# Performance work log

Hardware: AMD Instinct MI355X
Metric: run time of the kernel (lower is better)

## Reference

```python
import jax, jax.numpy as jnp
import numpy as np

B, S, D_IN, D_OUT, H = 2, 2048, 1024, 1024, 16
HD = D_OUT // H

def setup_inputs() -> dict:
    key = jax.random.key(0)
    ks = jax.random.split(key, 6)
    sc_in = 1.0 / np.sqrt(D_IN)
    sc_out = 1.0 / np.sqrt(D_OUT)
    return {
        "x": jax.random.normal(ks[0], (B, S, D_IN), dtype=jnp.float32),
        "Wq": jax.random.uniform(ks[1], (D_IN, D_OUT), jnp.float32, -sc_in, sc_in),
        "Wk": jax.random.uniform(ks[2], (D_IN, D_OUT), jnp.float32, -sc_in, sc_in),
        "Wv": jax.random.uniform(ks[3], (D_IN, D_OUT), jnp.float32, -sc_in, sc_in),
        "Wo": jax.random.uniform(ks[4], (D_OUT, D_OUT), jnp.float32, -sc_out, sc_out),
        "bo": jax.random.uniform(ks[5], (D_OUT,), jnp.float32, -sc_out, sc_out),
    }

def reference(x, Wq, Wk, Wv, Wo, bo):
    b, s, _ = x.shape
    # QKV projections (no bias), split heads -> [b, h, s, hd]
    q = (x @ Wq).reshape(b, s, H, HD).transpose(0, 2, 1, 3)
    k = (x @ Wk).reshape(b, s, H, HD).transpose(0, 2, 1, 3)
    v = (x @ Wv).reshape(b, s, H, HD).transpose(0, 2, 1, 3)
    scores = jnp.einsum('bhqd,bhkd->bhqk', q, k)
    causal = jnp.triu(jnp.ones((s, s), dtype=bool), k=1)
    scores = jnp.where(causal, -jnp.inf, scores)
    w = jax.nn.softmax(scores / np.sqrt(HD), axis=-1)  # dropout p=0.0 -> identity
    ctx = jnp.einsum('bhqk,bhkd->bhqd', w, v)
    ctx = ctx.transpose(0, 2, 1, 3).reshape(b, s, D_OUT)
    return ctx @ Wo + bo
```

## Files before the change

### kernel.cpp

```cpp
#include <hip/hip_runtime.h>
#include <stdint.h>

typedef unsigned short u16;
typedef __attribute__((ext_vector_type(8))) short short8;
typedef __attribute__((ext_vector_type(4))) float floatx4;
typedef __attribute__((ext_vector_type(4))) u16 ushort4v;

typedef __attribute__((address_space(1))) const uint32_t gu32;
typedef __attribute__((address_space(3))) uint32_t lu32;

#define MFMA(a, b, c) __builtin_amdgcn_mfma_f32_16x16x32_bf16((a), (b), (c), 0, 0, 0)

__device__ __forceinline__ u16 f2bf(float f) {
    union { float f; uint32_t u; } x; x.f = f;
    uint32_t u = x.u;
    u += 0x7fffu + ((u >> 16) & 1u);
    return (u16)(u >> 16);
}

__device__ __forceinline__ uint32_t cvtpk_bf16(float lo, float hi) {
    uint32_t r;
    asm("v_cvt_pk_bf16_f32 %0, %1, %2" : "=v"(r) : "v"(lo), "v"(hi));
    return r;
}

__device__ __forceinline__ float fexp2(float x) {
#if defined(__has_builtin)
#if __has_builtin(__builtin_amdgcn_exp2f)
    return __builtin_amdgcn_exp2f(x);
#else
    return exp2f(x);
#endif
#else
    return exp2f(x);
#endif
}

__device__ __forceinline__ void async16(u16* lds, const u16* g) {
    __builtin_amdgcn_global_load_lds((gu32*)g, (lu32*)lds, 16, 0, 0);
}

#define KV8(buf, row, byteInRow) \
    (*(short8*)((char*)(buf) + (((row) << 7) + ((byteInRow) ^ (((row) & 7) << 4)))))

#define Q_SCALE_LOG2E 0.18033688011112042f

__global__ __launch_bounds__(256) void prep_kernel(
    const float* __restrict__ x,
    const float* __restrict__ W0, const float* __restrict__ W1,
    const float* __restrict__ W2, const float* __restrict__ W3,
    u16* __restrict__ WT, u16* __restrict__ Xbf)
{
    const int z = blockIdx.z;
    const int tx = threadIdx.x, ty = threadIdx.y;
    if (z == 4) {
        const int bid = blockIdx.y * 32 + blockIdx.x;
        const int t = ty * 32 + tx;
        const size_t base = ((size_t)bid * 256 + t) * 16;
        const float* xf = x + base;
        short8 v0, v1;
#pragma unroll
        for (int j = 0; j < 8; j++) v0[j] = (short)f2bf(xf[j]);
#pragma unroll
        for (int j = 0; j < 8; j++) v1[j] = (short)f2bf(xf[8 + j]);
        *(short8*)&Xbf[base] = v0;
        *(short8*)&Xbf[base + 8] = v1;
        return;
    }
    __shared__ u16 tile[32][33];
    const float* W = (z == 0) ? W0 : (z == 1) ? W1 : (z == 2) ? W2 : W3;
    u16* dst = WT + (size_t)z * 1024 * 1024;
    const int n0 = blockIdx.x * 32, k0 = blockIdx.y * 32;
#pragma unroll
    for (int i = 0; i < 4; i++)
        tile[ty + i * 8][tx] = f2bf(W[(size_t)(k0 + ty + i * 8) * 1024 + n0 + tx]);
    __syncthreads();
#pragma unroll
    for (int i = 0; i < 4; i++)
        dst[(size_t)(n0 + ty + i * 8) * 1024 + k0 + tx] = tile[tx][ty + i * 8];
}

#define RSTAGE(Abuf, Bbuf, kk) do { \
    async16((Abuf) + (wave * 128) * 8,      gA0 + (kk)); \
    async16((Abuf) + (wave * 128 + 64) * 8, gA1 + (kk)); \
    async16((Bbuf) + (wave * 128) * 8,      gB0 + (kk)); \
    async16((Bbuf) + (wave * 128 + 64) * 8, gB1 + (kk)); \
} while (0)

#define GCOMPUTE(AB, BB) do { \
    short8 af[4], bfv[4]; \
    _Pragma("unroll") \
    for (int mt = 0; mt < 4; mt++) \
        af[mt] = *(const short8*)&(AB)[(wr + mt * 16 + lrow) * 32 + lquad * 8]; \
    _Pragma("unroll") \
    for (int nt = 0; nt < 4; nt++) \
        bfv[nt] = *(const short8*)&(BB)[(wc + nt * 16 + lrow) * 32 + lquad * 8]; \
    _Pragma("unroll") \
    for (int mt = 0; mt < 4; mt++) \
        _Pragma("unroll") \
        for (int nt = 0; nt < 4; nt++) \
            acc[mt][nt] = MFMA(af[mt], bfv[nt], acc[mt][nt]); \
} while (0)

#define RING_K_LOOP() do { \
    RSTAGE(As[0], Bs[0], 0); \
    RSTAGE(As[1], Bs[1], 32); \
    RSTAGE(As[2], Bs[2], 64); \
    for (int t = 0; t < 30; ++t) { \
        asm volatile("s_waitcnt vmcnt(8)" ::: "memory"); \
        __builtin_amdgcn_s_barrier(); \
        __builtin_amdgcn_sched_barrier(0); \
        if (t < 29) RSTAGE(As[(t + 3) & 3], Bs[(t + 3) & 3], (t + 3) * 32); \
        GCOMPUTE(As[t & 3], Bs[t & 3]); \
    } \
    asm volatile("s_waitcnt vmcnt(4)" ::: "memory"); \
    __builtin_amdgcn_s_barrier(); \
    __builtin_amdgcn_sched_barrier(0); \
    GCOMPUTE(As[2], Bs[2]); \
    asm volatile("s_waitcnt vmcnt(0)" ::: "memory"); \
    __builtin_amdgcn_s_barrier(); \
    __builtin_amdgcn_sched_barrier(0); \
    GCOMPUTE(As[3], Bs[3]); \
} while (0)

__global__ __launch_bounds__(256) void gemm_qkv_kernel(
    const u16* __restrict__ X, const u16* __restrict__ WT,
    u16* __restrict__ Q, u16* __restrict__ Kout, u16* __restrict__ VT)
{
    __shared__ __align__(16) u16 As[4][128 * 32];
    __shared__ __align__(16) u16 Bs[4][128 * 32];
    const int bid = blockIdx.x;
    const int xcd = bid & 7;
    const int idx = bid >> 3;
    const int mat = idx >> 5;
    const int rr  = (idx >> 3) & 3;
    const int nn  = idx & 7;
    const int m0 = (xcd * 4 + rr) * 128;
    const int n0 = nn * 128;
    const u16* BW = WT + (size_t)mat * 1024 * 1024;
    const int tid = threadIdx.x;
    const int wave = tid >> 6, lane = tid & 63;
    const int lrow = lane & 15, lquad = lane >> 4;
    const int wr = (wave >> 1) * 64, wc = (wave & 1) * 64;

    const int ci0 = wave * 128 + lane;
    const int ci1 = ci0 + 64;
    const int ar0 = ci0 >> 2, ac0 = (ci0 & 3) * 8;
    const int ar1 = ci1 >> 2, ac1 = (ci1 & 3) * 8;
    const u16* gA0 = &X[(size_t)(m0 + ar0) * 1024 + ac0];
    const u16* gA1 = &X[(size_t)(m0 + ar1) * 1024 + ac1];
    const u16* gB0 = &BW[(size_t)(n0 + ar0) * 1024 + ac0];
    const u16* gB1 = &BW[(size_t)(n0 + ar1) * 1024 + ac1];

    floatx4 acc[4][4];
#pragma unroll
    for (int mt = 0; mt < 4; mt++)
#pragma unroll
        for (int nt = 0; nt < 4; nt++) acc[mt][nt] = (floatx4){0.f, 0.f, 0.f, 0.f};

    RING_K_LOOP();

    const float qs = (mat == 0) ? Q_SCALE_LOG2E : 1.0f;
#pragma unroll
    for (int mt = 0; mt < 4; mt++) {
        const int gm = m0 + wr + mt * 16 + lquad * 4;
        const int b_ = gm >> 11;
        const int s  = gm & 2047;
#pragma unroll
        for (int nt = 0; nt < 4; nt++) {
            const int gn = n0 + wc + nt * 16 + lrow;
            const int h = gn >> 6, hd = gn & 63;
            const int bh = b_ * 16 + h;
            if (mat == 2) {
                ushort4v v;
#pragma unroll
                for (int i = 0; i < 4; i++) v[i] = f2bf(acc[mt][nt][i]);
                *(ushort4v*)&VT[((size_t)bh * 64 + hd) * 2048 + s] = v;
            } else {
                u16* dst = (mat == 0) ? Q : Kout;
#pragma unroll
                for (int i = 0; i < 4; i++)
                    dst[((size_t)bh * 2048 + s + i) * 64 + hd] = f2bf(acc[mt][nt][i] * qs);
            }
        }
    }
}

__global__ __launch_bounds__(256, 4) void attn_kernel(
    const u16* __restrict__ Q, const u16* __restrict__ Kk,
    const u16* __restrict__ VT, u16* __restrict__ ctx)
{
    __shared__ __align__(16) u16 Ks[64 * 64];
    __shared__ __align__(16) u16 Vs[64 * 64];
    __shared__ __align__(16) u16 P[4][16][80];
    const int tid = threadIdx.x, wave = tid >> 6, lane = tid & 63;
    const int lrow = lane & 15, lquad = lane >> 4;
    const float NEGINF = -__builtin_inff();

    const int bh = blockIdx.x & 31;
    const int g = blockIdx.x >> 5;
    const int qb = (g < 16) ? (31 - g) : (g - 16);
    const int ntiles = qb + 1;
    const int q0 = qb * 64 + wave * 16;

    const u16* Qb = Q  + (size_t)bh * 2048 * 64;
    const u16* Kb = Kk + (size_t)bh * 2048 * 64;
    const u16* Vb = VT + (size_t)bh * 64 * 2048;

    const short8 qf0 = *(const short8*)&Qb[(size_t)(q0 + lrow) * 64 + lquad * 8];
    const short8 qf1 = *(const short8*)&Qb[(size_t)(q0 + lrow) * 64 + 32 + lquad * 8];

    const int myq = q0 + lrow;
    float m_s = NEGINF, l_s = 0.f;
    floatx4 o[4];
#pragma unroll
    for (int i = 0; i < 4; i++) o[i] = (floatx4){0.f, 0.f, 0.f, 0.f};

    const int r0 = tid >> 3, r1 = r0 + 32;
    const int ce = (tid & 7) * 8;
    const int cb = (tid & 7) * 16;

    short8 kreg0 = *(const short8*)&Kb[(size_t)r0 * 64 + ce];
    short8 kreg1 = *(const short8*)&Kb[(size_t)r1 * 64 + ce];
    short8 vreg0 = *(const short8*)&Vb[(size_t)r0 * 2048 + ce];
    short8 vreg1 = *(const short8*)&Vb[(size_t)r1 * 2048 + ce];

    for (int kt = 0; kt < ntiles; kt++) {
        __syncthreads();
        KV8(Ks, r0, cb) = kreg0;
        KV8(Ks, r1, cb) = kreg1;
        KV8(Vs, r0, cb) = vreg0;
        KV8(Vs, r1, cb) = vreg1;
        if (kt + 1 < ntiles) {
            kreg0 = *(const short8*)&Kb[(size_t)((kt + 1) * 64 + r0) * 64 + ce];
            kreg1 = *(const short8*)&Kb[(size_t)((kt + 1) * 64 + r1) * 64 + ce];
            vreg0 = *(const short8*)&Vb[(size_t)r0 * 2048 + (kt + 1) * 64 + ce];
            vreg1 = *(const short8*)&Vb[(size_t)r1 * 2048 + (kt + 1) * 64 + ce];
        }
        __syncthreads();

        floatx4 s[4];
#pragma unroll
        for (int nt = 0; nt < 4; nt++) {
            const short8 kf0 = KV8(Ks, nt * 16 + lrow, lquad * 16);
            const short8 kf1 = KV8(Ks, nt * 16 + lrow, 64 + lquad * 16);
            floatx4 a = (floatx4){0.f, 0.f, 0.f, 0.f};
            a = MFMA(kf0, qf0, a);
            a = MFMA(kf1, qf1, a);
            s[nt] = a;
        }

        if (kt == ntiles - 1) {
#pragma unroll
            for (int nt = 0; nt < 4; nt++)
#pragma unroll
                for (int i = 0; i < 4; i++)
                    if (kt * 64 + nt * 16 + lquad * 4 + i > myq) s[nt][i] = NEGINF;
        }

        float mx = NEGINF;
#pragma unroll
        for (int nt = 0; nt < 4; nt++)
            mx = fmaxf(mx, fmaxf(fmaxf(s[nt][0], s[nt][1]),
                                 fmaxf(s[nt][2], s[nt][3])));
        mx = fmaxf(mx, __shfl_xor(mx, 16));
        mx = fmaxf(mx, __shfl_xor(mx, 32));

        if (!__all(mx <= m_s + 8.0f)) {
            const float mnew = fmaxf(m_s, mx);
            const float alpha = fexp2(m_s - mnew);
            m_s = mnew;
            l_s *= alpha;
#pragma unroll
            for (int ht = 0; ht < 4; ht++)
#pragma unroll
                for (int i = 0; i < 4; i++) o[ht][i] *= alpha;
        }

        float sum = 0.f;
#pragma unroll
        for (int nt = 0; nt < 4; nt++)
#pragma unroll
            for (int i = 0; i < 4; i++) {
                const float pv = fexp2(s[nt][i] - m_s);
                s[nt][i] = pv;
                sum += pv;
            }
        sum += __shfl_xor(sum, 16);
        sum += __shfl_xor(sum, 32);
        l_s += sum;

#pragma unroll
        for (int nt = 0; nt < 4; nt++) {
            uint2 pk;
            pk.x = cvtpk_bf16(s[nt][0], s[nt][1]);
            pk.y = cvtpk_bf16(s[nt][2], s[nt][3]);
            *(uint2*)&P[wave][lrow][nt * 16 + lquad * 4] = pk;
        }
#pragma unroll
        for (int st = 0; st < 2; st++) {
            const short8 pf = *(const short8*)&P[wave][lrow][st * 32 + lquad * 8];
#pragma unroll
            for (int ht = 0; ht < 4; ht++) {
                const short8 vf = KV8(Vs, ht * 16 + lrow, st * 64 + lquad * 16);
                o[ht] = MFMA(vf, pf, o[ht]);
            }
        }
    }

    const int b_ = bh >> 4, h_ = bh & 15;
    const float inv_l = 1.0f / l_s;
#pragma unroll
    for (int ht = 0; ht < 4; ht++) {
        uint2 pk;
        pk.x = cvtpk_bf16(o[ht][0] * inv_l, o[ht][1] * inv_l);
        pk.y = cvtpk_bf16(o[ht][2] * inv_l, o[ht][3] * inv_l);
        *(uint2*)&ctx[((size_t)(b_ * 2048 + q0 + lrow)) * 1024 + h_ * 64 + ht * 16 + lquad * 4] = pk;
    }
}

__global__ __launch_bounds__(256) void gemm_out_kernel(
    const u16* __restrict__ X, const u16* __restrict__ WT,
    const float* __restrict__ bias, float* __restrict__ out)
{
    __shared__ __align__(16) u16 As[4][128 * 32];
    __shared__ __align__(16) u16 Bs[4][128 * 32];
    const int bid = blockIdx.x;
    const int xcd = bid & 7;
    const int idx = bid >> 3;
    const int rr  = idx >> 3;
    const int nn  = idx & 7;
    const int m0 = (xcd * 4 + rr) * 128;
    const int n0 = nn * 128;
    const int tid = threadIdx.x;
    const int wave = tid >> 6, lane = tid & 63;
    const int lrow = lane & 15, lquad = lane >> 4;
    const int wr = (wave >> 1) * 64, wc = (wave & 1) * 64;

    const int ci0 = wave * 128 + lane;
    const int ci1 = ci0 + 64;
    const int ar0 = ci0 >> 2, ac0 = (ci0 & 3) * 8;
    const int ar1 = ci1 >> 2, ac1 = (ci1 & 3) * 8;
    const u16* gA0 = &X[(size_t)(m0 + ar0) * 1024 + ac0];
    const u16* gA1 = &X[(size_t)(m0 + ar1) * 1024 + ac1];
    const u16* gB0 = &WT[(size_t)(n0 + ar0) * 1024 + ac0];
    const u16* gB1 = &WT[(size_t)(n0 + ar1) * 1024 + ac1];

    floatx4 acc[4][4];
#pragma unroll
    for (int mt = 0; mt < 4; mt++)
#pragma unroll
        for (int nt = 0; nt < 4; nt++) acc[mt][nt] = (floatx4){0.f, 0.f, 0.f, 0.f};

    RING_K_LOOP();

#pragma unroll
    for (int mt = 0; mt < 4; mt++) {
        const int gm = m0 + wr + mt * 16 + lquad * 4;
#pragma unroll
        for (int nt = 0; nt < 4; nt++) {
            const int gn = n0 + wc + nt * 16 + lrow;
            const float bv = bias[gn];
#pragma unroll
            for (int i = 0; i < 4; i++)
                out[(size_t)(gm + i) * 1024 + gn] = acc[mt][nt][i] + bv;
        }
    }
}

extern "C" void kernel_launch(void* const* d_in, const int* in_sizes, int n_in,
                              void* d_out, int out_size, void* d_ws, size_t ws_size,
                              hipStream_t stream) {
    u16* ws = (u16*)d_ws + 64;

    const size_t MB1 = 1024 * 1024;
    u16* WT   = ws;
    u16* Qw   = ws + 4 * MB1;
    u16* Kw   = ws + 8 * MB1;
    u16* VTw  = ws + 12 * MB1;
    u16* ctxw = ws + 16 * MB1;
    u16* Xbf  = ws + 20 * MB1;

    prep_kernel<<<dim3(32, 32, 5), dim3(32, 8), 0, stream>>>(
        (const float*)d_in[0], (const float*)d_in[1], (const float*)d_in[2],
        (const float*)d_in[3], (const float*)d_in[4], WT, Xbf);
    gemm_qkv_kernel<<<768, 256, 0, stream>>>(Xbf, WT, Qw, Kw, VTw);
    attn_kernel<<<1024, 256, 0, stream>>>(Qw, Kw, VTw, ctxw);
    gemm_out_kernel<<<256, 256, 0, stream>>>(ctxw, WT + 3 * MB1, (const float*)d_in[5], (float*)d_out);
}
```

Before: 192.7 us.

## Enlarge QKV GEMM tiles to 256x256 with swizzled LDS and 8 waves

```diff
diff --git a/kernel.cpp b/kernel.cpp
--- a/kernel.cpp
+++ b/kernel.cpp
@@ -78,6 +78,263 @@
 #pragma unroll
     for (int i = 0; i < 4; i++)
         dst[(size_t)(n0 + ty + i * 8) * 1024 + k0 + tx] = tile[tx][ty + i * 8];
+}
+
+__global__ __launch_bounds__(512, 2) void gemm_qkv_kernel(
+    const u16* __restrict__ X, const u16* __restrict__ WT,
+    u16* __restrict__ Q, u16* __restrict__ Kout, u16* __restrict__ VT)
+{
+    __shared__ __align__(16) u16 As[4][256 * 32];
+    __shared__ __align__(16) u16 Bs[4][256 * 32];
+    const int bid = blockIdx.x;
+    const int xcd = bid & 7;
+    const int idx = bid >> 3;
+    const int rr  = idx & 1;
+    const int nn  = idx >> 1;
+    const int m0 = (xcd * 2 + rr) * 256;
+    const int n0 = nn * 256;
+    const int tid = threadIdx.x;
+    const int wave = tid >> 6, lane = tid & 63;
+    const int lrow = lane & 15, lquad = lane >> 4;
+    const int wr = (wave >> 2) * 128;
+    const int wc = (wave & 3) * 64;
+
+    const int c0 = wave * 128 + lane;
+    const int c1 = c0 + 64;
+    const int row0 = c0 >> 2, row1 = c1 >> 2;
+    const int gc0 = (((c0 & 3) ^ (row0 & 3)) * 8);
+    const int gc1 = (((c1 & 3) ^ (row1 & 3)) * 8);
+    const u16* gA0 = &X[(size_t)(m0 + row0) * 1024 + gc0];
+    const u16* gA1 = &X[(size_t)(m0 + row1) * 1024 + gc1];
+    const u16* gB0 = &WT[(size_t)(n0 + row0) * 1024 + gc0];
+    const u16* gB1 = &WT[(size_t)(n0 + row1) * 1024 + gc1];
+    const int ldsOff0 = (wave * 128) * 8;
+    const int ldsOff1 = (wave * 128 + 64) * 8;
+
+#define QSTAGE(b, kk) do { \
+    async16(&As[b][ldsOff0], gA0 + (kk)); \
+    async16(&As[b][ldsOff1], gA1 + (kk)); \
+    async16(&Bs[b][ldsOff0], gB0 + (kk)); \
+    async16(&Bs[b][ldsOff1], gB1 + (kk)); \
+} while (0)
+
+    const int sb = (lquad * 16) ^ ((lrow & 3) << 4);
+
+    floatx4 acc[8][4];
+#pragma unroll
+    for (int mt = 0; mt < 8; mt++)
+#pragma unroll
+        for (int nt = 0; nt < 4; nt++) acc[mt][nt] = (floatx4){0.f, 0.f, 0.f, 0.f};
+
+#define QCOMPUTE(b) do { \
+    const char* ab = (const char*)As[b]; \
+    const char* bb = (const char*)Bs[b]; \
+    short8 af[8], bf01[2], bf23[2]; \
+    _Pragma("unroll") \
+    for (int mt = 0; mt < 8; mt++) \
+        af[mt] = *(const short8*)(ab + (wr + mt * 16 + lrow) * 64 + sb); \
+    _Pragma("unroll") \
+    for (int nt = 0; nt < 2; nt++) \
+        bf01[nt] = *(const short8*)(bb + (wc + nt * 16 + lrow) * 64 + sb); \
+    __builtin_amdgcn_s_setprio(1); \
+    _Pragma("unroll") \
+    for (int mt = 0; mt < 8; mt++) { \
+        acc[mt][0] = MFMA(af[mt], bf01[0], acc[mt][0]); \
+        acc[mt][1] = MFMA(af[mt], bf01[1], acc[mt][1]); \
+    } \
+    __builtin_amdgcn_s_setprio(0); \
+    _Pragma("unroll") \
+    for (int nt = 0; nt < 2; nt++) \
+        bf23[nt] = *(const short8*)(bb + (wc + (nt + 2) * 16 + lrow) * 64 + sb); \
+    __builtin_amdgcn_s_setprio(1); \
+    _Pragma("unroll") \
+    for (int mt = 0; mt < 8; mt++) { \
+        acc[mt][2] = MFMA(af[mt], bf23[0], acc[mt][2]); \
+        acc[mt][3] = MFMA(af[mt], bf23[1], acc[mt][3]); \
+    } \
+    __builtin_amdgcn_s_setprio(0); \
+} while (0)
+
+    QSTAGE(0, 0);
+    QSTAGE(1, 32);
+    QSTAGE(2, 64);
+    for (int t = 0; t < 30; ++t) {
+        asm volatile("s_waitcnt vmcnt(8)" ::: "memory");
+        __builtin_amdgcn_s_barrier();
+        __builtin_amdgcn_sched_barrier(0);
+        if (t < 29) QSTAGE((t + 3) & 3, (t + 3) * 32);
+        QCOMPUTE(t & 3);
+    }
+    asm volatile("s_waitcnt vmcnt(4)" ::: "memory");
+    __builtin_amdgcn_s_barrier();
+    __builtin_amdgcn_sched_barrier(0);
+    QCOMPUTE(2);
+    asm volatile("s_waitcnt vmcnt(0)" ::: "memory");
+    __builtin_amdgcn_s_barrier();
+    __builtin_amdgcn_sched_barrier(0);
+    QCOMPUTE(3);
+
+#undef QSTAGE
+#undef QCOMPUTE
+
+    const int mat = n0 >> 10;
+    const float qs = (mat == 0) ? Q_SCALE_LOG2E : 1.0f;
+#pragma unroll
+    for (int mt = 0; mt < 8; mt++) {
+        const int gm = m0 + wr + mt * 16 + lquad * 4;
+        const int b_ = gm >> 11;
+        const int s  = gm & 2047;
+#pragma unroll
+        for (int nt = 0; nt < 4; nt++) {
+            const int gn = n0 + wc + nt * 16 + lrow;
+            const int h = (gn & 1023) >> 6, hd = gn & 63;
+            const int bh = b_ * 16 + h;
+            if (mat == 2) {
+                ushort4v v;
+#pragma unroll
+                for (int i = 0; i < 4; i++) v[i] = f2bf(acc[mt][nt][i]);
+                *(ushort4v*)&VT[((size_t)bh * 64 + hd) * 2048 + s] = v;
+            } else {
+                u16* dst = (mat == 0) ? Q : Kout;
+#pragma unroll
+                for (int i = 0; i < 4; i++)
+                    dst[((size_t)bh * 2048 + s + i) * 64 + hd] = f2bf(acc[mt][nt][i] * qs);
+            }
+        }
+    }
+}
+
+__global__ __launch_bounds__(256, 4) void attn_kernel(
+    const u16* __restrict__ Q, const u16* __restrict__ Kk,
+    const u16* __restrict__ VT, u16* __restrict__ ctx)
+{
+    __shared__ __align__(16) u16 Ks[64 * 64];
+    __shared__ __align__(16) u16 Vs[64 * 64];
+    __shared__ __align__(16) u16 P[4][16][80];
+    const int tid = threadIdx.x, wave = tid >> 6, lane = tid & 63;
+    const int lrow = lane & 15, lquad = lane >> 4;
+    const float NEGINF = -__builtin_inff();
+
+    const int bh = blockIdx.x & 31;
+    const int g = blockIdx.x >> 5;
+    const int qb = (g < 16) ? (31 - g) : (g - 16);
+    const int ntiles = qb + 1;
+    const int q0 = qb * 64 + wave * 16;
+
+    const u16* Qb = Q  + (size_t)bh * 2048 * 64;
+    const u16* Kb = Kk + (size_t)bh * 2048 * 64;
+    const u16* Vb = VT + (size_t)bh * 64 * 2048;
+
+    const short8 qf0 = *(const short8*)&Qb[(size_t)(q0 + lrow) * 64 + lquad * 8];
+    const short8 qf1 = *(const short8*)&Qb[(size_t)(q0 + lrow) * 64 + 32 + lquad * 8];
+
+    const int myq = q0 + lrow;
+    float m_s = NEGINF, l_s = 0.f;
+    floatx4 o[4];
+#pragma unroll
+    for (int i = 0; i < 4; i++) o[i] = (floatx4){0.f, 0.f, 0.f, 0.f};
+
+    const int r0 = tid >> 3, r1 = r0 + 32;
+    const int ce = (tid & 7) * 8;
+    const int cb = (tid & 7) * 16;
+
+    short8 kreg0 = *(const short8*)&Kb[(size_t)r0 * 64 + ce];
+    short8 kreg1 = *(const short8*)&Kb[(size_t)r1 * 64 + ce];
+    short8 vreg0 = *(const short8*)&Vb[(size_t)r0 * 2048 + ce];
+    short8 vreg1 = *(const short8*)&Vb[(size_t)r1 * 2048 + ce];
+
+    for (int kt = 0; kt < ntiles; kt++) {
+        __syncthreads();
+        KV8(Ks, r0, cb) = kreg0;
+        KV8(Ks, r1, cb) = kreg1;
+        KV8(Vs, r0, cb) = vreg0;
+        KV8(Vs, r1, cb) = vreg1;
+        if (kt + 1 < ntiles) {
+            kreg0 = *(const short8*)&Kb[(size_t)((kt + 1) * 64 + r0) * 64 + ce];
+            kreg1 = *(const short8*)&Kb[(size_t)((kt + 1) * 64 + r1) * 64 + ce];
+            vreg0 = *(const short8*)&Vb[(size_t)r0 * 2048 + (kt + 1) * 64 + ce];
+            vreg1 = *(const short8*)&Vb[(size_t)r1 * 2048 + (kt + 1) * 64 + ce];
+        }
+        __syncthreads();
+
+        floatx4 s[4];
+#pragma unroll
+        for (int nt = 0; nt < 4; nt++) {
+            const short8 kf0 = KV8(Ks, nt * 16 + lrow, lquad * 16);
+            const short8 kf1 = KV8(Ks, nt * 16 + lrow, 64 + lquad * 16);
+            floatx4 a = (floatx4){0.f, 0.f, 0.f, 0.f};
+            a = MFMA(kf0, qf0, a);
+            a = MFMA(kf1, qf1, a);
+            s[nt] = a;
+        }
+
+        if (kt == ntiles - 1) {
+#pragma unroll
+            for (int nt = 0; nt < 4; nt++)
+#pragma unroll
+                for (int i = 0; i < 4; i++)
+                    if (kt * 64 + nt * 16 + lquad * 4 + i > myq) s[nt][i] = NEGINF;
+        }
+
+        float mx = NEGINF;
+#pragma unroll
+        for (int nt = 0; nt < 4; nt++)
+            mx = fmaxf(mx, fmaxf(fmaxf(s[nt][0], s[nt][1]),
+                                 fmaxf(s[nt][2], s[nt][3])));
+        mx = fmaxf(mx, __shfl_xor(mx, 16));
+        mx = fmaxf(mx, __shfl_xor(mx, 32));
+
+        if (!__all(mx <= m_s + 8.0f)) {
+            const float mnew = fmaxf(m_s, mx);
+            const float alpha = fexp2(m_s - mnew);
+            m_s = mnew;
+            l_s *= alpha;
+#pragma unroll
+            for (int ht = 0; ht < 4; ht++)
+#pragma unroll
+                for (int i = 0; i < 4; i++) o[ht][i] *= alpha;
+        }
+
+        float sum = 0.f;
+#pragma unroll
+        for (int nt = 0; nt < 4; nt++)
+#pragma unroll
+            for (int i = 0; i < 4; i++) {
+                const float pv = fexp2(s[nt][i] - m_s);
+                s[nt][i] = pv;
+                sum += pv;
+            }
+        sum += __shfl_xor(sum, 16);
+        sum += __shfl_xor(sum, 32);
+        l_s += sum;
+
+#pragma unroll
+        for (int nt = 0; nt < 4; nt++) {
+            uint2 pk;
+            pk.x = cvtpk_bf16(s[nt][0], s[nt][1]);
+            pk.y = cvtpk_bf16(s[nt][2], s[nt][3]);
+            *(uint2*)&P[wave][lrow][nt * 16 + lquad * 4] = pk;
+        }
+#pragma unroll
+        for (int st = 0; st < 2; st++) {
+            const short8 pf = *(const short8*)&P[wave][lrow][st * 32 + lquad * 8];
+#pragma unroll
+            for (int ht = 0; ht < 4; ht++) {
+                const short8 vf = KV8(Vs, ht * 16 + lrow, st * 64 + lquad * 16);
+                o[ht] = MFMA(vf, pf, o[ht]);
+            }
+        }
+    }
+
+    const int b_ = bh >> 4, h_ = bh & 15;
+    const float inv_l = 1.0f / l_s;
+#pragma unroll
+    for (int ht = 0; ht < 4; ht++) {
+        uint2 pk;
+        pk.x = cvtpk_bf16(o[ht][0] * inv_l, o[ht][1] * inv_l);
+        pk.y = cvtpk_bf16(o[ht][2] * inv_l, o[ht][3] * inv_l);
+        *(uint2*)&ctx[((size_t)(b_ * 2048 + q0 + lrow)) * 1024 + h_ * 64 + ht * 16 + lquad * 4] = pk;
+    }
 }
 
 #define RSTAGE(Abuf, Bbuf, kk) do { \
@@ -123,202 +380,6 @@
     GCOMPUTE(As[3], Bs[3]); \
 } while (0)
 
-__global__ __launch_bounds__(256) void gemm_qkv_kernel(
-    const u16* __restrict__ X, const u16* __restrict__ WT,
-    u16* __restrict__ Q, u16* __restrict__ Kout, u16* __restrict__ VT)
-{
-    __shared__ __align__(16) u16 As[4][128 * 32];
-    __shared__ __align__(16) u16 Bs[4][128 * 32];
-    const int bid = blockIdx.x;
-    const int xcd = bid & 7;
-    const int idx = bid >> 3;
-    const int mat = idx >> 5;
-    const int rr  = (idx >> 3) & 3;
-    const int nn  = idx & 7;
-    const int m0 = (xcd * 4 + rr) * 128;
-    const int n0 = nn * 128;
-    const u16* BW = WT + (size_t)mat * 1024 * 1024;
-    const int tid = threadIdx.x;
-    const int wave = tid >> 6, lane = tid & 63;
-    const int lrow = lane & 15, lquad = lane >> 4;
-    const int wr = (wave >> 1) * 64, wc = (wave & 1) * 64;
-
-    const int ci0 = wave * 128 + lane;
-    const int ci1 = ci0 + 64;
-    const int ar0 = ci0 >> 2, ac0 = (ci0 & 3) * 8;
-    const int ar1 = ci1 >> 2, ac1 = (ci1 & 3) * 8;
-    const u16* gA0 = &X[(size_t)(m0 + ar0) * 1024 + ac0];
-    const u16* gA1 = &X[(size_t)(m0 + ar1) * 1024 + ac1];
-    const u16* gB0 = &BW[(size_t)(n0 + ar0) * 1024 + ac0];
-    const u16* gB1 = &BW[(size_t)(n0 + ar1) * 1024 + ac1];
-
-    floatx4 acc[4][4];
-#pragma unroll
-    for (int mt = 0; mt < 4; mt++)
-#pragma unroll
-        for (int nt = 0; nt < 4; nt++) acc[mt][nt] = (floatx4){0.f, 0.f, 0.f, 0.f};
-
-    RING_K_LOOP();
-
-    const float qs = (mat == 0) ? Q_SCALE_LOG2E : 1.0f;
-#pragma unroll
-    for (int mt = 0; mt < 4; mt++) {
-        const int gm = m0 + wr + mt * 16 + lquad * 4;
-        const int b_ = gm >> 11;
-        const int s  = gm & 2047;
-#pragma unroll
-        for (int nt = 0; nt < 4; nt++) {
-            const int gn = n0 + wc + nt * 16 + lrow;
-            const int h = gn >> 6, hd = gn & 63;
-            const int bh = b_ * 16 + h;
-            if (mat == 2) {
-                ushort4v v;
-#pragma unroll
-                for (int i = 0; i < 4; i++) v[i] = f2bf(acc[mt][nt][i]);
-                *(ushort4v*)&VT[((size_t)bh * 64 + hd) * 2048 + s] = v;
-            } else {
-                u16* dst = (mat == 0) ? Q : Kout;
-#pragma unroll
-                for (int i = 0; i < 4; i++)
-                    dst[((size_t)bh * 2048 + s + i) * 64 + hd] = f2bf(acc[mt][nt][i] * qs);
-            }
-        }
-    }
-}
-
-__global__ __launch_bounds__(256, 4) void attn_kernel(
-    const u16* __restrict__ Q, const u16* __restrict__ Kk,
-    const u16* __restrict__ VT, u16* __restrict__ ctx)
-{
-    __shared__ __align__(16) u16 Ks[64 * 64];
-    __shared__ __align__(16) u16 Vs[64 * 64];
-    __shared__ __align__(16) u16 P[4][16][80];
-    const int tid = threadIdx.x, wave = tid >> 6, lane = tid & 63;
-    const int lrow = lane & 15, lquad = lane >> 4;
-    const float NEGINF = -__builtin_inff();
-
-    const int bh = blockIdx.x & 31;
-    const int g = blockIdx.x >> 5;
-    const int qb = (g < 16) ? (31 - g) : (g - 16);
-    const int ntiles = qb + 1;
-    const int q0 = qb * 64 + wave * 16;
-
-    const u16* Qb = Q  + (size_t)bh * 2048 * 64;
-    const u16* Kb = Kk + (size_t)bh * 2048 * 64;
-    const u16* Vb = VT + (size_t)bh * 64 * 2048;
-
-    const short8 qf0 = *(const short8*)&Qb[(size_t)(q0 + lrow) * 64 + lquad * 8];
-    const short8 qf1 = *(const short8*)&Qb[(size_t)(q0 + lrow) * 64 + 32 + lquad * 8];
-
-    const int myq = q0 + lrow;
-    float m_s = NEGINF, l_s = 0.f;
-    floatx4 o[4];
-#pragma unroll
-    for (int i = 0; i < 4; i++) o[i] = (floatx4){0.f, 0.f, 0.f, 0.f};
-
-    const int r0 = tid >> 3, r1 = r0 + 32;
-    const int ce = (tid & 7) * 8;
-    const int cb = (tid & 7) * 16;
-
-    short8 kreg0 = *(const short8*)&Kb[(size_t)r0 * 64 + ce];
-    short8 kreg1 = *(const short8*)&Kb[(size_t)r1 * 64 + ce];
-    short8 vreg0 = *(const short8*)&Vb[(size_t)r0 * 2048 + ce];
-    short8 vreg1 = *(const short8*)&Vb[(size_t)r1 * 2048 + ce];
-
-    for (int kt = 0; kt < ntiles; kt++) {
-        __syncthreads();
-        KV8(Ks, r0, cb) = kreg0;
-        KV8(Ks, r1, cb) = kreg1;
-        KV8(Vs, r0, cb) = vreg0;
-        KV8(Vs, r1, cb) = vreg1;
-        if (kt + 1 < ntiles) {
-            kreg0 = *(const short8*)&Kb[(size_t)((kt + 1) * 64 + r0) * 64 + ce];
-            kreg1 = *(const short8*)&Kb[(size_t)((kt + 1) * 64 + r1) * 64 + ce];
-            vreg0 = *(const short8*)&Vb[(size_t)r0 * 2048 + (kt + 1) * 64 + ce];
-            vreg1 = *(const short8*)&Vb[(size_t)r1 * 2048 + (kt + 1) * 64 + ce];
-        }
-        __syncthreads();
-
-        floatx4 s[4];
-#pragma unroll
-        for (int nt = 0; nt < 4; nt++) {
-            const short8 kf0 = KV8(Ks, nt * 16 + lrow, lquad * 16);
-            const short8 kf1 = KV8(Ks, nt * 16 + lrow, 64 + lquad * 16);
-            floatx4 a = (floatx4){0.f, 0.f, 0.f, 0.f};
-            a = MFMA(kf0, qf0, a);
-            a = MFMA(kf1, qf1, a);
-            s[nt] = a;
-        }
-
-        if (kt == ntiles - 1) {
-#pragma unroll
-            for (int nt = 0; nt < 4; nt++)
-#pragma unroll
-                for (int i = 0; i < 4; i++)
-                    if (kt * 64 + nt * 16 + lquad * 4 + i > myq) s[nt][i] = NEGINF;
-        }
-
-        float mx = NEGINF;
-#pragma unroll
-        for (int nt = 0; nt < 4; nt++)
-            mx = fmaxf(mx, fmaxf(fmaxf(s[nt][0], s[nt][1]),
-                                 fmaxf(s[nt][2], s[nt][3])));
-        mx = fmaxf(mx, __shfl_xor(mx, 16));
-        mx = fmaxf(mx, __shfl_xor(mx, 32));
-
-        if (!__all(mx <= m_s + 8.0f)) {
-            const float mnew = fmaxf(m_s, mx);
-            const float alpha = fexp2(m_s - mnew);
-            m_s = mnew;
-            l_s *= alpha;
-#pragma unroll
-            for (int ht = 0; ht < 4; ht++)
-#pragma unroll
-                for (int i = 0; i < 4; i++) o[ht][i] *= alpha;
-        }
-
-        float sum = 0.f;
-#pragma unroll
-        for (int nt = 0; nt < 4; nt++)
-#pragma unroll
-            for (int i = 0; i < 4; i++) {
-                const float pv = fexp2(s[nt][i] - m_s);
-                s[nt][i] = pv;
-                sum += pv;
-            }
-        sum += __shfl_xor(sum, 16);
-        sum += __shfl_xor(sum, 32);
-        l_s += sum;
-
-#pragma unroll
-        for (int nt = 0; nt < 4; nt++) {
-            uint2 pk;
-            pk.x = cvtpk_bf16(s[nt][0], s[nt][1]);
-            pk.y = cvtpk_bf16(s[nt][2], s[nt][3]);
-            *(uint2*)&P[wave][lrow][nt * 16 + lquad * 4] = pk;
-        }
-#pragma unroll
-        for (int st = 0; st < 2; st++) {
-            const short8 pf = *(const short8*)&P[wave][lrow][st * 32 + lquad * 8];
-#pragma unroll
-            for (int ht = 0; ht < 4; ht++) {
-                const short8 vf = KV8(Vs, ht * 16 + lrow, st * 64 + lquad * 16);
-                o[ht] = MFMA(vf, pf, o[ht]);
-            }
-        }
-    }
-
-    const int b_ = bh >> 4, h_ = bh & 15;
-    const float inv_l = 1.0f / l_s;
-#pragma unroll
-    for (int ht = 0; ht < 4; ht++) {
-        uint2 pk;
-        pk.x = cvtpk_bf16(o[ht][0] * inv_l, o[ht][1] * inv_l);
-        pk.y = cvtpk_bf16(o[ht][2] * inv_l, o[ht][3] * inv_l);
-        *(uint2*)&ctx[((size_t)(b_ * 2048 + q0 + lrow)) * 1024 + h_ * 64 + ht * 16 + lquad * 4] = pk;
-    }
-}
-
 __global__ __launch_bounds__(256) void gemm_out_kernel(
     const u16* __restrict__ X, const u16* __restrict__ WT,
     const float* __restrict__ bias, float* __restrict__ out)
@@ -384,7 +445,7 @@
     prep_kernel<<<dim3(32, 32, 5), dim3(32, 8), 0, stream>>>(
         (const float*)d_in[0], (const float*)d_in[1], (const float*)d_in[2],
         (const float*)d_in[3], (const float*)d_in[4], WT, Xbf);
-    gemm_qkv_kernel<<<768, 256, 0, stream>>>(Xbf, WT, Qw, Kw, VTw);
+    gemm_qkv_kernel<<<192, 512, 0, stream>>>(Xbf, WT, Qw, Kw, VTw);
     attn_kernel<<<1024, 256, 0, stream>>>(Qw, Kw, VTw, ctxw);
     gemm_out_kernel<<<256, 256, 0, stream>>>(ctxw, WT + 3 * MB1, (const float*)d_in[5], (float*)d_out);
 }
```

Result: no change. 194.8 us (+1.1%).

## Replace 4-stage async ring with single-buffer BK=64 swizzled GEMM loop

Applied to the files above, without the earlier changes.

```diff
diff --git a/kernel.cpp b/kernel.cpp
--- a/kernel.cpp
+++ b/kernel.cpp
@@ -80,55 +80,47 @@
         dst[(size_t)(n0 + ty + i * 8) * 1024 + k0 + tx] = tile[tx][ty + i * 8];
 }
 
-#define RSTAGE(Abuf, Bbuf, kk) do { \
-    async16((Abuf) + (wave * 128) * 8,      gA0 + (kk)); \
-    async16((Abuf) + (wave * 128 + 64) * 8, gA1 + (kk)); \
-    async16((Bbuf) + (wave * 128) * 8,      gB0 + (kk)); \
-    async16((Bbuf) + (wave * 128 + 64) * 8, gB1 + (kk)); \
+#define GSTAGE64(buf, gptr, kk) do { \
+    _Pragma("unroll") \
+    for (int i_ = 0; i_ < 4; i_++) \
+        async16((buf) + wave * 512 + i_ * 2048, (gptr) + (kk) + (size_t)i_ * 32 * 1024); \
 } while (0)
 
-#define GCOMPUTE(AB, BB) do { \
-    short8 af[4], bfv[4]; \
+#define GFRAG64(buf, base, ks, fr) \
+    (*(const short8*)&(buf)[((base) + (fr) * 16 + lrow) * 64 + ((((ks) * 4 + lquad) ^ (lrow & 7)) * 8)])
+
+#define GCOMPUTE64() do { \
     _Pragma("unroll") \
-    for (int mt = 0; mt < 4; mt++) \
-        af[mt] = *(const short8*)&(AB)[(wr + mt * 16 + lrow) * 32 + lquad * 8]; \
-    _Pragma("unroll") \
-    for (int nt = 0; nt < 4; nt++) \
-        bfv[nt] = *(const short8*)&(BB)[(wc + nt * 16 + lrow) * 32 + lquad * 8]; \
-    _Pragma("unroll") \
-    for (int mt = 0; mt < 4; mt++) \
+    for (int ks = 0; ks < 2; ks++) { \
+        short8 af[4], bfv[4]; \
         _Pragma("unroll") \
-        for (int nt = 0; nt < 4; nt++) \
-            acc[mt][nt] = MFMA(af[mt], bfv[nt], acc[mt][nt]); \
+        for (int mt = 0; mt < 4; mt++) af[mt] = GFRAG64(As, wr, ks, mt); \
+        _Pragma("unroll") \
+        for (int nt = 0; nt < 4; nt++) bfv[nt] = GFRAG64(Bs, wc, ks, nt); \
+        _Pragma("unroll") \
+        for (int mt = 0; mt < 4; mt++) \
+            _Pragma("unroll") \
+            for (int nt = 0; nt < 4; nt++) \
+                acc[mt][nt] = MFMA(af[mt], bfv[nt], acc[mt][nt]); \
+    } \
 } while (0)
 
-#define RING_K_LOOP() do { \
-    RSTAGE(As[0], Bs[0], 0); \
-    RSTAGE(As[1], Bs[1], 32); \
-    RSTAGE(As[2], Bs[2], 64); \
-    for (int t = 0; t < 30; ++t) { \
-        asm volatile("s_waitcnt vmcnt(8)" ::: "memory"); \
-        __builtin_amdgcn_s_barrier(); \
-        __builtin_amdgcn_sched_barrier(0); \
-        if (t < 29) RSTAGE(As[(t + 3) & 3], Bs[(t + 3) & 3], (t + 3) * 32); \
-        GCOMPUTE(As[t & 3], Bs[t & 3]); \
+#define GEMM_K_LOOP64() do { \
+    for (int kk = 0; kk < 1024; kk += 64) { \
+        __syncthreads(); \
+        GSTAGE64(As, gA, kk); \
+        GSTAGE64(Bs, gB, kk); \
+        __syncthreads(); \
+        GCOMPUTE64(); \
     } \
-    asm volatile("s_waitcnt vmcnt(4)" ::: "memory"); \
-    __builtin_amdgcn_s_barrier(); \
-    __builtin_amdgcn_sched_barrier(0); \
-    GCOMPUTE(As[2], Bs[2]); \
-    asm volatile("s_waitcnt vmcnt(0)" ::: "memory"); \
-    __builtin_amdgcn_s_barrier(); \
-    __builtin_amdgcn_sched_barrier(0); \
-    GCOMPUTE(As[3], Bs[3]); \
 } while (0)
 
 __global__ __launch_bounds__(256) void gemm_qkv_kernel(
     const u16* __restrict__ X, const u16* __restrict__ WT,
     u16* __restrict__ Q, u16* __restrict__ Kout, u16* __restrict__ VT)
 {
-    __shared__ __align__(16) u16 As[4][128 * 32];
-    __shared__ __align__(16) u16 Bs[4][128 * 32];
+    __shared__ __align__(16) u16 As[128 * 64];
+    __shared__ __align__(16) u16 Bs[128 * 64];
     const int bid = blockIdx.x;
     const int xcd = bid & 7;
     const int idx = bid >> 3;
@@ -143,14 +135,10 @@
     const int lrow = lane & 15, lquad = lane >> 4;
     const int wr = (wave >> 1) * 64, wc = (wave & 1) * 64;
 
-    const int ci0 = wave * 128 + lane;
-    const int ci1 = ci0 + 64;
-    const int ar0 = ci0 >> 2, ac0 = (ci0 & 3) * 8;
-    const int ar1 = ci1 >> 2, ac1 = (ci1 & 3) * 8;
-    const u16* gA0 = &X[(size_t)(m0 + ar0) * 1024 + ac0];
-    const u16* gA1 = &X[(size_t)(m0 + ar1) * 1024 + ac1];
-    const u16* gB0 = &BW[(size_t)(n0 + ar0) * 1024 + ac0];
-    const u16* gB1 = &BW[(size_t)(n0 + ar1) * 1024 + ac1];
+    const int stg_r = tid >> 3;
+    const int stg_c = ((tid & 7) ^ ((tid >> 3) & 7)) * 8;
+    const u16* gA = &X[(size_t)(m0 + stg_r) * 1024 + stg_c];
+    const u16* gB = &BW[(size_t)(n0 + stg_r) * 1024 + stg_c];
 
     floatx4 acc[4][4];
 #pragma unroll
@@ -158,7 +146,7 @@
 #pragma unroll
         for (int nt = 0; nt < 4; nt++) acc[mt][nt] = (floatx4){0.f, 0.f, 0.f, 0.f};
 
-    RING_K_LOOP();
+    GEMM_K_LOOP64();
 
     const float qs = (mat == 0) ? Q_SCALE_LOG2E : 1.0f;
 #pragma unroll
@@ -323,8 +311,8 @@
     const u16* __restrict__ X, const u16* __restrict__ WT,
     const float* __restrict__ bias, float* __restrict__ out)
 {
-    __shared__ __align__(16) u16 As[4][128 * 32];
-    __shared__ __align__(16) u16 Bs[4][128 * 32];
+    __shared__ __align__(16) u16 As[128 * 64];
+    __shared__ __align__(16) u16 Bs[128 * 64];
     const int bid = blockIdx.x;
     const int xcd = bid & 7;
     const int idx = bid >> 3;
@@ -337,14 +325,10 @@
     const int lrow = lane & 15, lquad = lane >> 4;
     const int wr = (wave >> 1) * 64, wc = (wave & 1) * 64;
 
-    const int ci0 = wave * 128 + lane;
-    const int ci1 = ci0 + 64;
-    const int ar0 = ci0 >> 2, ac0 = (ci0 & 3) * 8;
-    const int ar1 = ci1 >> 2, ac1 = (ci1 & 3) * 8;
-    const u16* gA0 = &X[(size_t)(m0 + ar0) * 1024 + ac0];
-    const u16* gA1 = &X[(size_t)(m0 + ar1) * 1024 + ac1];
-    const u16* gB0 = &WT[(size_t)(n0 + ar0) * 1024 + ac0];
-    const u16* gB1 = &WT[(size_t)(n0 + ar1) * 1024 + ac1];
+    const int stg_r = tid >> 3;
+    const int stg_c = ((tid & 7) ^ ((tid >> 3) & 7)) * 8;
+    const u16* gA = &X[(size_t)(m0 + stg_r) * 1024 + stg_c];
+    const u16* gB = &WT[(size_t)(n0 + stg_r) * 1024 + stg_c];
 
     floatx4 acc[4][4];
 #pragma unroll
@@ -352,7 +336,7 @@
 #pragma unroll
         for (int nt = 0; nt < 4; nt++) acc[mt][nt] = (floatx4){0.f, 0.f, 0.f, 0.f};
 
-    RING_K_LOOP();
+    GEMM_K_LOOP64();
 
 #pragma unroll
     for (int mt = 0; mt < 4; mt++) {
```

New measurement: 180.7 us. 1.07x faster.
